# Kernel optimization log

Measured on AMD Instinct MI355X. Metric: run time of the kernel, lower is better.

The kernel has to match this reference:

```python
import jax, jax.numpy as jnp
import numpy as np

EPS = 1e-12  # F.normalize default eps


def setup_inputs() -> dict:
    key = jax.random.key(0)
    k1, k2, k3, k4 = jax.random.split(key, 4)
    B, C, H, W = 8, 256, 128, 128
    N, T = 100, 6
    return {
        "visual_features": jax.random.normal(k1, (B, C, H, W), dtype=jnp.float32),
        "text_embeddings": jax.random.normal(k2, (T, C), dtype=jnp.float32),
        "masks": jax.random.uniform(k3, (B, N, H, W), dtype=jnp.float32),
        "class_labels": jax.random.randint(k4, (B, N), 0, 7),
        "temperature": jnp.asarray(0.07, dtype=jnp.float32),
    }


def reference(visual_features, text_embeddings, masks, class_labels, temperature):
    # visual_features: (B,C,H,W); text_embeddings: (T,C); masks: (B,N,H,W); class_labels: (B,N)
    T = text_embeddings.shape[0]
    # masks already at (H,W): bilinear resize to same size is identity -> just threshold
    mask_bin = (masks > 0.5).astype(visual_features.dtype)          # (B,N,H,W), detached
    mask_bin = jax.lax.stop_gradient(mask_bin)
    msum = mask_bin.sum(axis=(2, 3))                                 # (B,N)
    # masked sum-pool then mean (clamp denom at 1, as in torch)
    pooled = jnp.einsum('bchw,bnhw->bnc', visual_features, mask_bin)
    pooled = pooled / jnp.maximum(msum, 1.0)[..., None]              # (B,N,C)
    pooled = pooled / jnp.maximum(jnp.linalg.norm(pooled, axis=-1, keepdims=True), EPS)
    text_norm = text_embeddings / jnp.maximum(
        jnp.linalg.norm(text_embeddings, axis=-1, keepdims=True), EPS)
    sims = jnp.einsum('bnc,tc->bnt', pooled, text_norm) / jnp.abs(temperature)  # (B,N,T)
    logp = jax.nn.log_softmax(sims, axis=-1)
    tgt = jnp.clip(class_labels - 1, 0, T - 1)
    ce = -jnp.take_along_axis(logp, tgt[..., None], axis=-1)[..., 0]  # (B,N)
    valid = ((class_labels >= 1) & (class_labels <= T) & (msum >= 1.0)).astype(ce.dtype)
    cnt = valid.sum()
    loss = jnp.where(cnt > 0, (ce * valid).sum() / jnp.maximum(cnt, 1.0),
                     jnp.asarray(0.0, ce.dtype))
    return loss
```

## Files before the change

kernel.cpp:

```cpp
#include <hip/hip_runtime.h>
#include <hip/hip_bf16.h>
#include <stdint.h>

constexpr int cB  = 8;
constexpr int cC  = 256;
constexpr int cHW = 128 * 128;
constexpr int cN  = 100;
constexpr int cT  = 6;
constexpr int NPAD = 112;
constexpr int WPB = cHW / 32;
constexpr int KSLICES = 32;
constexpr int PXS = cHW / KSLICES;
constexpr int NWIN = PXS / 32;
constexpr int NGRP = NWIN / 4;
constexpr int NBLK = cB * 16 * (KSLICES / 4);
constexpr int FINBLK = cB * cN / 4;

typedef __attribute__((ext_vector_type(8))) short short8;
typedef __attribute__((ext_vector_type(4))) float floatx4;

__device__ __forceinline__ unsigned pack2(float a, float b) {
    const __hip_bfloat16 ha = __float2bfloat16(a);
    const __hip_bfloat16 hb = __float2bfloat16(b);
    return (unsigned)__builtin_bit_cast(unsigned short, ha)
         | ((unsigned)__builtin_bit_cast(unsigned short, hb) << 16);
}

__device__ __forceinline__ float wred(float v) {
    #pragma unroll
    for (int off = 32; off > 0; off >>= 1) v += __shfl_xor(v, off, 64);
    return v;
}

__global__ __launch_bounds__(256)
void mask_prep_kernel(const float* __restrict__ masks, const float* __restrict__ text,
                      unsigned* __restrict__ bits, unsigned* __restrict__ msum,
                      float* __restrict__ tnorm)
{
    const int t = threadIdx.x, lane = t & 63, w = t >> 6;

    if (blockIdx.x == cB * NPAD) {
        float v[cT], sq[cT];
        #pragma unroll
        for (int q = 0; q < cT; ++q) {
            v[q] = text[q * cC + t];
            sq[q] = wred(v[q] * v[q]);
        }
        __shared__ float ps[cT][4];
        if (lane == 0)
            #pragma unroll
            for (int q = 0; q < cT; ++q) ps[q][w] = sq[q];
        __syncthreads();
        #pragma unroll
        for (int q = 0; q < cT; ++q) {
            const float nrm = fmaxf(sqrtf(ps[q][0] + ps[q][1] + ps[q][2] + ps[q][3]), 1e-12f);
            tnorm[q * cC + t] = v[q] / nrm;
        }
        return;
    }

    const int b = blockIdx.x / NPAD;
    const int n = blockIdx.x % NPAD;
    unsigned* dst = bits + ((size_t)b * NPAD + n) * WPB;
    if (n >= cN) { *(uint2*)(dst + t * 2) = make_uint2(0u, 0u); return; }

    const float* src = masks + ((size_t)b * cN + n) * cHW + w * 4096;
    unsigned* wdst = dst + w * 128;
    int pc = 0;
    #pragma unroll
    for (int r = 0; r < 16; ++r) {
        const floatx4 v = *(const floatx4*)(src + r * 256 + lane * 4);
        const bool b0 = v.x > 0.5f, b1 = v.y > 0.5f, b2 = v.z > 0.5f, b3 = v.w > 0.5f;
        const unsigned long long B0 = __ballot(b0), B1 = __ballot(b1),
                                 B2 = __ballot(b2), B3 = __ballot(b3);
        pc += (int)b0 + (int)b1 + (int)b2 + (int)b3;
        if (lane < 8) {
            const int sh = lane * 8;
            const unsigned word =
                  (unsigned)((B0 >> sh) & 0xFFull)
                | ((unsigned)((B1 >> sh) & 0xFFull) << 8)
                | ((unsigned)((B2 >> sh) & 0xFFull) << 16)
                | ((unsigned)((B3 >> sh) & 0xFFull) << 24);
            wdst[r * 8 + lane] = word;
        }
    }
    #pragma unroll
    for (int off = 32; off > 0; off >>= 1) pc += __shfl_xor(pc, off, 64);
    __shared__ int ps2[4];
    if (lane == 0) ps2[w] = pc;
    __syncthreads();
    if (t == 0) msum[b * cN + n] = (unsigned)(ps2[0] + ps2[1] + ps2[2] + ps2[3]);
}

__global__ __launch_bounds__(256)
void pool_kernel(const float* __restrict__ vf, const unsigned* __restrict__ bits,
                 float* __restrict__ part)
{
    __shared__ float red[4][28][64];

    const int tid  = threadIdx.x;
    const int lane = tid & 63;
    const int widx = tid >> 6;
    const int bid  = blockIdx.x;
    const int b    = bid >> 7;
    const int ct   = (bid >> 3) & 15;
    const int kg   = bid & 7;
    const int sl   = kg * 4 + widx;
    const int l15  = lane & 15;
    const int lk   = lane >> 4;
    const int lk2  = lk * 2;
    const int p0   = sl * PXS;

    const float* vrow = vf + ((size_t)(b * cC + ct * 16 + l15)) * cHW + p0 + lk * 8;
    const unsigned* brow = bits + ((size_t)b * NPAD + l15) * WPB + (p0 >> 5);

    floatx4 acc[7];
    #pragma unroll
    for (int mt = 0; mt < 7; ++mt) acc[mt] = (floatx4){0.f, 0.f, 0.f, 0.f};

    floatx4 vr[4][2];
    #pragma unroll
    for (int u = 0; u < 4; ++u) {
        vr[u][0] = *(const floatx4*)(vrow + u * 32);
        vr[u][1] = *(const floatx4*)(vrow + u * 32 + 4);
    }
    uint4 bwA[7], bwB[7];
    #pragma unroll
    for (int mt = 0; mt < 7; ++mt)
        bwA[mt] = *(const uint4*)(brow + (size_t)mt * 16 * WPB);

    auto GROUP = [&](int g, uint4 (&bw)[7], uint4 (&bwn)[7]) {
        if (g < NGRP - 1) {
            #pragma unroll
            for (int mt = 0; mt < 7; ++mt)
                bwn[mt] = *(const uint4*)(brow + (size_t)mt * 16 * WPB + (g + 1) * 4);
        }
        #pragma unroll
        for (int u = 0; u < 4; ++u) {
            const int w = g * 4 + u;
            union { short8 s8; uint4 u4; } bq;
            bq.u4.x = pack2(vr[u][0].x, vr[u][0].y);
            bq.u4.y = pack2(vr[u][0].z, vr[u][0].w);
            bq.u4.z = pack2(vr[u][1].x, vr[u][1].y);
            bq.u4.w = pack2(vr[u][1].z, vr[u][1].w);
            if (g < NGRP - 1) {
                vr[u][0] = *(const floatx4*)(vrow + (w + 4) * 32);
                vr[u][1] = *(const floatx4*)(vrow + (w + 4) * 32 + 4);
            }
            #pragma unroll
            for (int mt = 0; mt < 7; ++mt) {
                const unsigned word = (u == 0) ? bw[mt].x : (u == 1) ? bw[mt].y
                                    : (u == 2) ? bw[mt].z : bw[mt].w;
                const unsigned te = (word >> lk2) & 0x01010101u;
                const unsigned to = (word >> (lk2 + 1)) & 0x01010101u;
                union { short8 s8; uint4 u4; } aq;
                aq.u4.x = __umul24(__builtin_amdgcn_perm(0u, te, 0x04010400u), 0x3F80u);
                aq.u4.y = __umul24(__builtin_amdgcn_perm(0u, te, 0x04030402u), 0x3F80u);
                aq.u4.z = __umul24(__builtin_amdgcn_perm(0u, to, 0x04010400u), 0x3F80u);
                aq.u4.w = __umul24(__builtin_amdgcn_perm(0u, to, 0x04030402u), 0x3F80u);
                acc[mt] = __builtin_amdgcn_mfma_f32_16x16x32_bf16(aq.s8, bq.s8, acc[mt], 0, 0, 0);
            }
        }
    };

    GROUP(0, bwA, bwB);
    GROUP(1, bwB, bwA);
    GROUP(2, bwA, bwB);
    GROUP(3, bwB, bwA);

    #pragma unroll
    for (int mt = 0; mt < 7; ++mt)
        #pragma unroll
        for (int i = 0; i < 4; ++i)
            red[widx][mt * 4 + i][lane] = acc[mt][i];
    __syncthreads();

    float s[7];
    #pragma unroll
    for (int mt = 0; mt < 7; ++mt) {
        const int e = mt * 4 + widx;
        s[mt] = red[0][e][lane] + red[1][e][lane] + red[2][e][lane] + red[3][e][lane];
    }
    float* dst = part + (size_t)bid * (cN * 16);
    #pragma unroll
    for (int mt = 0; mt < 7; ++mt) {
        const int n = mt * 16 + (lane >> 4) * 4 + widx;
        if (n < cN) dst[n * 16 + l15] = s[mt];
    }
}

__global__ __launch_bounds__(256)
void finalize_kernel(const float* __restrict__ part, const unsigned* __restrict__ msum,
                     const float* __restrict__ tnorm, const int* __restrict__ labels,
                     const float* __restrict__ temp, float* __restrict__ bpart)
{
    const int tid  = threadIdx.x;
    const int lane = tid & 63;
    const int wv   = tid >> 6;
    const int row  = blockIdx.x * 4 + wv;
    const int b = row / cN, n = row % cN;
    const int ct  = lane >> 2;
    const int col = (lane & 3) * 4;
    const int c_global = ct * 16 + col;

    floatx4 p = (floatx4){0.f, 0.f, 0.f, 0.f};
    const float* src = part + ((size_t)(b * 128 + ct * 8)) * (cN * 16) + n * 16 + col;
    #pragma unroll
    for (int g = 0; g < 8; ++g)
        p += *(const floatx4*)(src + (size_t)g * (cN * 16));

    const float m   = (float)msum[row];
    const float inv = 1.0f / fmaxf(m, 1.0f);
    p.x *= inv; p.y *= inv; p.z *= inv; p.w *= inv;

    float psq = p.x * p.x + p.y * p.y + p.z * p.z + p.w * p.w;
    float dot[cT];
    #pragma unroll
    for (int q = 0; q < cT; ++q) {
        const floatx4 x = *(const floatx4*)(tnorm + (size_t)q * cC + c_global);
        dot[q] = p.x * x.x + p.y * x.y + p.z * x.z + p.w * x.w;
    }
    psq = wred(psq);
    #pragma unroll
    for (int q = 0; q < cT; ++q) dot[q] = wred(dot[q]);

    __shared__ float lce[4], lcnt[4];
    if (lane == 0) {
        const float tempv = fabsf(temp[0]);
        const float pn = fmaxf(sqrtf(psq), 1e-12f);
        float sims[cT], mx = -1e30f;
        #pragma unroll
        for (int q = 0; q < cT; ++q) {
            sims[q] = dot[q] / pn / tempv;
            mx = fmaxf(mx, sims[q]);
        }
        float se = 0.f;
        #pragma unroll
        for (int q = 0; q < cT; ++q) se += expf(sims[q] - mx);
        const float lse = logf(se);

        const int lab = labels[row];
        const int tgt = min(max(lab - 1, 0), cT - 1);
        const float ce = -(sims[tgt] - mx - lse);
        const bool valid = (lab >= 1) && (lab <= cT) && (m >= 1.0f);
        lce[wv]  = valid ? ce : 0.f;
        lcnt[wv] = valid ? 1.f : 0.f;
    }
    __syncthreads();
    if (tid == 0) {
        bpart[blockIdx.x * 2]     = lce[0] + lce[1] + lce[2] + lce[3];
        bpart[blockIdx.x * 2 + 1] = lcnt[0] + lcnt[1] + lcnt[2] + lcnt[3];
    }
}

__global__ __launch_bounds__(256)
void loss_kernel(const float* __restrict__ bp, float* __restrict__ out) {
    const int t = threadIdx.x, lane = t & 63, w = t >> 6;
    float ce = 0.f, cnt = 0.f;
    if (t < FINBLK) { ce = bp[t * 2]; cnt = bp[t * 2 + 1]; }
    ce = wred(ce); cnt = wred(cnt);
    __shared__ float a[8];
    if (lane == 0) { a[w * 2] = ce; a[w * 2 + 1] = cnt; }
    __syncthreads();
    if (t == 0) {
        const float s = a[0] + a[2] + a[4] + a[6];
        const float c = a[1] + a[3] + a[5] + a[7];
        out[0] = (c > 0.f) ? s / fmaxf(c, 1.f) : 0.f;
    }
}

extern "C" void kernel_launch(void* const* d_in, const int* in_sizes, int n_in,
                              void* d_out, int out_size, void* d_ws, size_t ws_size,
                              hipStream_t stream)
{
    const float* vf     = (const float*)d_in[0];
    const float* text   = (const float*)d_in[1];
    const float* masks  = (const float*)d_in[2];
    const int*   labels = (const int*)d_in[3];
    const float* temp   = (const float*)d_in[4];

    float*    wsf    = (float*)d_ws;
    float*    bpart  = wsf;
    float*    tnorm  = wsf + 512;
    unsigned* msum   = (unsigned*)(wsf + 2048);
    float*    part   = wsf + 4096;
    const size_t PART_FLOATS = (size_t)NBLK * cN * 16;
    const size_t BITS_WORDS  = (size_t)cB * NPAD * WPB;
    unsigned* bits   = (unsigned*)(wsf + 4096 + PART_FLOATS);

    if (ws_size < (4096 + PART_FLOATS + BITS_WORDS + 64) * sizeof(float))
        return;

    hipLaunchKernelGGL(mask_prep_kernel, dim3(cB * NPAD + 1), dim3(256), 0, stream,
                       masks, text, bits, msum, tnorm);
    hipLaunchKernelGGL(pool_kernel, dim3(NBLK), dim3(256), 0, stream,
                       vf, bits, part);
    hipLaunchKernelGGL(finalize_kernel, dim3(FINBLK), dim3(256), 0, stream,
                       part, msum, tnorm, labels, temp, bpart);
    hipLaunchKernelGGL(loss_kernel, dim3(1), dim3(256), 0, stream,
                       bpart, (float*)d_out);
}
```

Before: 53.70 us.

## Fuse mask binarization into pooling kernel with per-chunk shared-memory bitmasks

Merges the mask thresholding/bit-packing kernel into the MFMA pooling kernel. Each 1024-thread block handles one batch and a 512-pixel chunk: it thresholds all 100 masks for that chunk into LDS bits and per-chunk counts, then 16 waves each cover 16 channels. This removes the global bitmask round-trip and one launch. In exchange the partial buffer grows (32 chunks x 16 channel tiles), finalize must sum 32 partials and reduce per-chunk mask counts, and only 257 large blocks are launched, with each block's mask load serialized before its MFMA phase.

```diff
diff --git a/kernel.cpp b/kernel.cpp
--- a/kernel.cpp
+++ b/kernel.cpp
@@ -8,12 +8,11 @@
 constexpr int cN  = 100;
 constexpr int cT  = 6;
 constexpr int NPAD = 112;
-constexpr int WPB = cHW / 32;
-constexpr int KSLICES = 32;
-constexpr int PXS = cHW / KSLICES;
-constexpr int NWIN = PXS / 32;
-constexpr int NGRP = NWIN / 4;
-constexpr int NBLK = cB * 16 * (KSLICES / 4);
+constexpr int CHUNK  = 512;
+constexpr int NCHUNK = cHW / CHUNK;
+constexpr int PBLK   = cB * NCHUNK;
+constexpr int NWIN   = CHUNK / 32;
+constexpr int NGRP   = NWIN / 4;
 constexpr int FINBLK = cB * cN / 4;
 
 typedef __attribute__((ext_vector_type(8))) short short8;
@@ -32,87 +31,95 @@
     return v;
 }
 
-__global__ __launch_bounds__(256)
-void mask_prep_kernel(const float* __restrict__ masks, const float* __restrict__ text,
-                      unsigned* __restrict__ bits, unsigned* __restrict__ msum,
-                      float* __restrict__ tnorm)
+__global__ __launch_bounds__(1024)
+void fused_pool_kernel(const float* __restrict__ vf, const float* __restrict__ masks,
+                       const float* __restrict__ text,
+                       float* __restrict__ part, float* __restrict__ msump,
+                       float* __restrict__ tnorm)
 {
-    const int t = threadIdx.x, lane = t & 63, w = t >> 6;
-
-    if (blockIdx.x == cB * NPAD) {
-        float v[cT], sq[cT];
-        #pragma unroll
-        for (int q = 0; q < cT; ++q) {
-            v[q] = text[q * cC + t];
-            sq[q] = wred(v[q] * v[q]);
-        }
-        __shared__ float ps[cT][4];
-        if (lane == 0)
-            #pragma unroll
-            for (int q = 0; q < cT; ++q) ps[q][w] = sq[q];
-        __syncthreads();
-        #pragma unroll
-        for (int q = 0; q < cT; ++q) {
-            const float nrm = fmaxf(sqrtf(ps[q][0] + ps[q][1] + ps[q][2] + ps[q][3]), 1e-12f);
-            tnorm[q * cC + t] = v[q] / nrm;
-        }
-        return;
-    }
-
-    const int b = blockIdx.x / NPAD;
-    const int n = blockIdx.x % NPAD;
-    unsigned* dst = bits + ((size_t)b * NPAD + n) * WPB;
-    if (n >= cN) { *(uint2*)(dst + t * 2) = make_uint2(0u, 0u); return; }
-
-    const float* src = masks + ((size_t)b * cN + n) * cHW + w * 4096;
-    unsigned* wdst = dst + w * 128;
-    int pc = 0;
-    #pragma unroll
-    for (int r = 0; r < 16; ++r) {
-        const floatx4 v = *(const floatx4*)(src + r * 256 + lane * 4);
-        const bool b0 = v.x > 0.5f, b1 = v.y > 0.5f, b2 = v.z > 0.5f, b3 = v.w > 0.5f;
-        const unsigned long long B0 = __ballot(b0), B1 = __ballot(b1),
-                                 B2 = __ballot(b2), B3 = __ballot(b3);
-        pc += (int)b0 + (int)b1 + (int)b2 + (int)b3;
-        if (lane < 8) {
-            const int sh = lane * 8;
-            const unsigned word =
-                  (unsigned)((B0 >> sh) & 0xFFull)
-                | ((unsigned)((B1 >> sh) & 0xFFull) << 8)
-                | ((unsigned)((B2 >> sh) & 0xFFull) << 16)
-                | ((unsigned)((B3 >> sh) & 0xFFull) << 24);
-            wdst[r * 8 + lane] = word;
-        }
-    }
-    #pragma unroll
-    for (int off = 32; off > 0; off >>= 1) pc += __shfl_xor(pc, off, 64);
-    __shared__ int ps2[4];
-    if (lane == 0) ps2[w] = pc;
-    __syncthreads();
-    if (t == 0) msum[b * cN + n] = (unsigned)(ps2[0] + ps2[1] + ps2[2] + ps2[3]);
-}
-
-__global__ __launch_bounds__(256)
-void pool_kernel(const float* __restrict__ vf, const unsigned* __restrict__ bits,
-                 float* __restrict__ part)
-{
-    __shared__ float red[4][28][64];
-
     const int tid  = threadIdx.x;
     const int lane = tid & 63;
-    const int widx = tid >> 6;
-    const int bid  = blockIdx.x;
-    const int b    = bid >> 7;
-    const int ct   = (bid >> 3) & 15;
-    const int kg   = bid & 7;
-    const int sl   = kg * 4 + widx;
-    const int l15  = lane & 15;
-    const int lk   = lane >> 4;
-    const int lk2  = lk * 2;
-    const int p0   = sl * PXS;
-
-    const float* vrow = vf + ((size_t)(b * cC + ct * 16 + l15)) * cHW + p0 + lk * 8;
-    const unsigned* brow = bits + ((size_t)b * NPAD + l15) * WPB + (p0 >> 5);
+    const int w    = tid >> 6;
+
+    if (blockIdx.x == PBLK) {
+        __shared__ float ps[cT][4];
+        float v[cT], sq[cT];
+        if (tid < 256) {
+            #pragma unroll
+            for (int q = 0; q < cT; ++q) {
+                v[q] = text[q * cC + tid];
+                sq[q] = wred(v[q] * v[q]);
+            }
+            if (lane == 0)
+                #pragma unroll
+                for (int q = 0; q < cT; ++q) ps[q][w] = sq[q];
+        }
+        __syncthreads();
+        if (tid < 256) {
+            #pragma unroll
+            for (int q = 0; q < cT; ++q) {
+                const float nrm = fmaxf(sqrtf(ps[q][0] + ps[q][1] + ps[q][2] + ps[q][3]), 1e-12f);
+                tnorm[q * cC + tid] = v[q] / nrm;
+            }
+        }
+        return;
+    }
+
+    __shared__ unsigned bitsL[NPAD][NWIN];
+    __shared__ float    msum_f[NPAD];
+
+    const int bid   = blockIdx.x;
+    const int b     = bid >> 5;
+    const int chunk = bid & 31;
+    const int p0    = chunk * CHUNK;
+
+    if (tid < (NPAD - cN) * NWIN)
+        (&bitsL[0][0])[cN * NWIN + tid] = 0u;
+
+    {
+        const float* mbase = masks + (size_t)b * cN * cHW + p0;
+        int n = w;
+        floatx4 m0 = *(const floatx4*)(mbase + (size_t)n * cHW + lane * 4);
+        floatx4 m1 = *(const floatx4*)(mbase + (size_t)n * cHW + 256 + lane * 4);
+        while (true) {
+            const int n2 = n + 16;
+            floatx4 m0n, m1n;
+            if (n2 < cN) {
+                m0n = *(const floatx4*)(mbase + (size_t)n2 * cHW + lane * 4);
+                m1n = *(const floatx4*)(mbase + (size_t)n2 * cHW + 256 + lane * 4);
+            }
+            int pc = 0;
+            #pragma unroll
+            for (int p = 0; p < 2; ++p) {
+                const floatx4 v = p ? m1 : m0;
+                const bool b0 = v.x > 0.5f, b1 = v.y > 0.5f, b2 = v.z > 0.5f, b3 = v.w > 0.5f;
+                const unsigned long long B0 = __ballot(b0), B1 = __ballot(b1),
+                                         B2 = __ballot(b2), B3 = __ballot(b3);
+                pc += __popcll(B0) + __popcll(B1) + __popcll(B2) + __popcll(B3);
+                if (lane < 8) {
+                    const int sh = lane * 8;
+                    const unsigned word =
+                          (unsigned)((B0 >> sh) & 0xFFull)
+                        | ((unsigned)((B1 >> sh) & 0xFFull) << 8)
+                        | ((unsigned)((B2 >> sh) & 0xFFull) << 16)
+                        | ((unsigned)((B3 >> sh) & 0xFFull) << 24);
+                    bitsL[n][p * 8 + lane] = word;
+                }
+            }
+            if (lane == 0) msum_f[n] = (float)pc;
+            if (n2 >= cN) break;
+            n = n2; m0 = m0n; m1 = m1n;
+        }
+    }
+    __syncthreads();
+
+    if (tid < cN) msump[(size_t)bid * NPAD + tid] = msum_f[tid];
+
+    const int l15 = lane & 15;
+    const int lk  = lane >> 4;
+    const int lk2 = lk * 2;
+
+    const float* vrow = vf + ((size_t)(b * cC + w * 16 + l15)) * cHW + p0 + lk * 8;
 
     floatx4 acc[7];
     #pragma unroll
@@ -124,28 +131,24 @@
         vr[u][0] = *(const floatx4*)(vrow + u * 32);
         vr[u][1] = *(const floatx4*)(vrow + u * 32 + 4);
     }
-    uint4 bwA[7], bwB[7];
-    #pragma unroll
-    for (int mt = 0; mt < 7; ++mt)
-        bwA[mt] = *(const uint4*)(brow + (size_t)mt * 16 * WPB);
-
-    auto GROUP = [&](int g, uint4 (&bw)[7], uint4 (&bwn)[7]) {
-        if (g < NGRP - 1) {
-            #pragma unroll
-            for (int mt = 0; mt < 7; ++mt)
-                bwn[mt] = *(const uint4*)(brow + (size_t)mt * 16 * WPB + (g + 1) * 4);
-        }
+
+    #pragma unroll
+    for (int g = 0; g < NGRP; ++g) {
+        uint4 bw[7];
+        #pragma unroll
+        for (int mt = 0; mt < 7; ++mt)
+            bw[mt] = *(const uint4*)&bitsL[mt * 16 + l15][g * 4];
         #pragma unroll
         for (int u = 0; u < 4; ++u) {
-            const int w = g * 4 + u;
+            const int win = g * 4 + u;
             union { short8 s8; uint4 u4; } bq;
             bq.u4.x = pack2(vr[u][0].x, vr[u][0].y);
             bq.u4.y = pack2(vr[u][0].z, vr[u][0].w);
             bq.u4.z = pack2(vr[u][1].x, vr[u][1].y);
             bq.u4.w = pack2(vr[u][1].z, vr[u][1].w);
             if (g < NGRP - 1) {
-                vr[u][0] = *(const floatx4*)(vrow + (w + 4) * 32);
-                vr[u][1] = *(const floatx4*)(vrow + (w + 4) * 32 + 4);
+                vr[u][0] = *(const floatx4*)(vrow + (win + 4) * 32);
+                vr[u][1] = *(const floatx4*)(vrow + (win + 4) * 32 + 4);
             }
             #pragma unroll
             for (int mt = 0; mt < 7; ++mt) {
@@ -161,36 +164,21 @@
                 acc[mt] = __builtin_amdgcn_mfma_f32_16x16x32_bf16(aq.s8, bq.s8, acc[mt], 0, 0, 0);
             }
         }
-    };
-
-    GROUP(0, bwA, bwB);
-    GROUP(1, bwB, bwA);
-    GROUP(2, bwA, bwB);
-    GROUP(3, bwB, bwA);
-
-    #pragma unroll
-    for (int mt = 0; mt < 7; ++mt)
-        #pragma unroll
-        for (int i = 0; i < 4; ++i)
-            red[widx][mt * 4 + i][lane] = acc[mt][i];
-    __syncthreads();
-
-    float s[7];
+    }
+
+    float* dst = part + (size_t)(bid * 16 + w) * (cN * 16);
     #pragma unroll
     for (int mt = 0; mt < 7; ++mt) {
-        const int e = mt * 4 + widx;
-        s[mt] = red[0][e][lane] + red[1][e][lane] + red[2][e][lane] + red[3][e][lane];
-    }
-    float* dst = part + (size_t)bid * (cN * 16);
-    #pragma unroll
-    for (int mt = 0; mt < 7; ++mt) {
-        const int n = mt * 16 + (lane >> 4) * 4 + widx;
-        if (n < cN) dst[n * 16 + l15] = s[mt];
+        #pragma unroll
+        for (int i = 0; i < 4; ++i) {
+            const int n = mt * 16 + lk * 4 + i;
+            if (n < cN) dst[n * 16 + l15] = acc[mt][i];
+        }
     }
 }
 
 __global__ __launch_bounds__(256)
-void finalize_kernel(const float* __restrict__ part, const unsigned* __restrict__ msum,
+void finalize_kernel(const float* __restrict__ part, const float* __restrict__ msump,
                      const float* __restrict__ tnorm, const int* __restrict__ labels,
                      const float* __restrict__ temp, float* __restrict__ bpart)
 {
@@ -204,12 +192,13 @@
     const int c_global = ct * 16 + col;
 
     floatx4 p = (floatx4){0.f, 0.f, 0.f, 0.f};
-    const float* src = part + ((size_t)(b * 128 + ct * 8)) * (cN * 16) + n * 16 + col;
-    #pragma unroll
-    for (int g = 0; g < 8; ++g)
-        p += *(const floatx4*)(src + (size_t)g * (cN * 16));
-
-    const float m   = (float)msum[row];
+    const float* src = part + ((size_t)(b * NCHUNK * 16 + ct)) * (cN * 16) + n * 16 + col;
+    #pragma unroll
+    for (int ch = 0; ch < NCHUNK; ++ch)
+        p += *(const floatx4*)(src + (size_t)ch * 16 * (cN * 16));
+
+    const float m = wred(lane < NCHUNK
+                         ? msump[(size_t)(b * NCHUNK + lane) * NPAD + n] : 0.f);
     const float inv = 1.0f / fmaxf(m, 1.0f);
     p.x *= inv; p.y *= inv; p.z *= inv; p.w *= inv;
 
@@ -279,24 +268,20 @@
     const int*   labels = (const int*)d_in[3];
     const float* temp   = (const float*)d_in[4];
 
-    float*    wsf    = (float*)d_ws;
-    float*    bpart  = wsf;
-    float*    tnorm  = wsf + 512;
-    unsigned* msum   = (unsigned*)(wsf + 2048);
-    float*    part   = wsf + 4096;
-    const size_t PART_FLOATS = (size_t)NBLK * cN * 16;
-    const size_t BITS_WORDS  = (size_t)cB * NPAD * WPB;
-    unsigned* bits   = (unsigned*)(wsf + 4096 + PART_FLOATS);
-
-    if (ws_size < (4096 + PART_FLOATS + BITS_WORDS + 64) * sizeof(float))
+    float* wsf   = (float*)d_ws;
+    float* bpart = wsf;
+    float* tnorm = wsf + 512;
+    float* msump = wsf + 2048;
+    float* part  = wsf + 32768;
+    const size_t PART_FLOATS = (size_t)PBLK * 16 * cN * 16;
+
+    if (ws_size < (32768 + PART_FLOATS + 64) * sizeof(float))
         return;
 
-    hipLaunchKernelGGL(mask_prep_kernel, dim3(cB * NPAD + 1), dim3(256), 0, stream,
-                       masks, text, bits, msum, tnorm);
-    hipLaunchKernelGGL(pool_kernel, dim3(NBLK), dim3(256), 0, stream,
-                       vf, bits, part);
+    hipLaunchKernelGGL(fused_pool_kernel, dim3(PBLK + 1), dim3(1024), 0, stream,
+                       vf, masks, text, part, msump, tnorm);
     hipLaunchKernelGGL(finalize_kernel, dim3(FINBLK), dim3(256), 0, stream,
-                       part, msum, tnorm, labels, temp, bpart);
+                       part, msump, tnorm, labels, temp, bpart);
     hipLaunchKernelGGL(loss_kernel, dim3(1), dim3(256), 0, stream,
                        bpart, (float*)d_out);
 }
```

Result: faster. 47.20 us (-12.1%).
